# Kernel optimization log

Hardware: AMD Instinct MI355X
Metric: run time of the kernel (lower is better)

The kernel has to match this reference:

```python
import jax, jax.numpy as jnp
import numpy as np

B, H, S, D = 2, 16, 2048, 64


def setup_inputs() -> dict:
    key = jax.random.key(0)
    kq, kk, kv = jax.random.split(key, 3)
    Q = jax.random.normal(kq, (B, H, S, D), dtype=jnp.float32)
    K = jax.random.normal(kk, (B, H, S, D), dtype=jnp.float32)
    V = jax.random.normal(kv, (B, H, S, D), dtype=jnp.float32)
    # causal mask: True = masked out (matches torch masked_fill_ semantics)
    causal = ~jnp.tril(jnp.ones((S, S), dtype=bool))
    mask = jnp.broadcast_to(causal, (B, H, S, S))
    return {"Q": Q, "K": K, "V": V, "mask": mask}


def reference(Q, K, V, mask):
    d_q = Q.shape[-1]
    scale = 1.0 / np.sqrt(d_q).astype(np.float32)
    # scores: (B, H, S, S)
    scores = jnp.einsum('bhqd,bhkd->bhqk', Q, K) * scale
    scores = jnp.where(mask, jnp.float32(-1e9), scores)
    attention = jax.nn.softmax(scores, axis=-1)
    context = jnp.einsum('bhqk,bhkd->bhqd', attention, V)
    return (context, attention)
```

## Files before the change

### kernel.cpp

```cpp
#include <hip/hip_runtime.h>
#include <hip/hip_bf16.h>


constexpr int SEQ = 2048;
constexpr int HD  = 64;
constexpr int NHEADS = 32;
constexpr int QT  = 64;
constexpr int NT  = SEQ / QT;

typedef __bf16 bf16x8 __attribute__((ext_vector_type(8)));
typedef unsigned short u16x8 __attribute__((ext_vector_type(8)));
typedef unsigned short u16x4 __attribute__((ext_vector_type(4)));
typedef float f32x4 __attribute__((ext_vector_type(4)));
typedef unsigned short us;

__device__ __forceinline__ us f2bf(float x) {
  unsigned u = __builtin_bit_cast(unsigned, x);
  return (us)((u + 0x7fffu + ((u >> 16) & 1u)) >> 16);
}
__device__ __forceinline__ float bf2f(us b) {
  return __builtin_bit_cast(float, (unsigned)b << 16);
}

__launch_bounds__(256, 2)
__global__ void attn_kernel(const float* __restrict__ Qg,
                            const float* __restrict__ Kg,
                            const float* __restrict__ Vg,
                            float* __restrict__ out) {
  const int fb = blockIdx.x;
  const int bh = fb & (NHEADS - 1);
  const int pi = fb >> 5;
  const int t  = threadIdx.x;
  const int l  = t & 63;
  const int w  = t >> 6;
  const int l16 = l & 15;
  const int lg  = l >> 4;

  __shared__ __align__(16) us Qs[QT * HD];
  __shared__ __align__(16) us Ks[QT * HD];
  __shared__ __align__(16) us Vs[QT * HD];
  __shared__ __align__(16) us Ps[4][16 * QT];

  const size_t hoff = (size_t)bh * SEQ * HD;
  const float* Qh = Qg + hoff;
  const float* Kh = Kg + hoff;
  const float* Vh = Vg + hoff;
  float* ctx = out + hoff;
  float* att = out + (size_t)NHEADS * SEQ * HD + (size_t)bh * SEQ * SEQ;

  auto load_tile = [&](const float* src, f32x4 (&reg)[4]) {
    #pragma unroll
    for (int j = 0; j < 4; ++j) {
      const int f = t + 256 * j;
      reg[j] = *(const f32x4*)(src + (size_t)(f >> 4) * HD + 4 * (f & 15));
    }
  };
  auto write_k = [&](const f32x4 (&reg)[4], us* dst) {
    #pragma unroll
    for (int j = 0; j < 4; ++j) {
      const int f = t + 256 * j;
      const int r = f >> 4, c4 = f & 15;
      const int idx = (r * 64 + 4 * c4) ^ ((r & 7) << 3);
      u16x4 b = { f2bf(reg[j].x), f2bf(reg[j].y), f2bf(reg[j].z), f2bf(reg[j].w) };
      *(u16x4*)(&dst[idx]) = b;
    }
  };
  auto write_vv = [&](const f32x4 (&reg)[4], us* dst) {
    #pragma unroll
    for (int j = 0; j < 4; ++j) {
      const int f = t + 256 * j;
      const int r = f >> 4, c4 = f & 15;
      const int idx = (r * 64 + 4 * c4) ^ (((r >> 3) & 3) << 4);
      u16x4 b = { f2bf(reg[j].x), f2bf(reg[j].y), f2bf(reg[j].z), f2bf(reg[j].w) };
      *(u16x4*)(&dst[idx]) = b;
    }
  };

  const float sc = 0.125f;

  for (int half = 0; half < 2; ++half) {
    const int qt = half ? (NT - 1 - pi) : pi;
    const int qbase = qt * QT;
    const int qg = qbase + w * 16 + l16;

    __syncthreads();

    {
      const int zc0 = (qt + 1) * QT;
      const int nz4 = (SEQ - zc0) >> 2;
      for (int r = 0; r < QT; ++r) {
        float* rowp = att + (size_t)(qbase + r) * SEQ + zc0;
        for (int c = t; c < nz4; c += 256)
          __builtin_nontemporal_store((f32x4){0.f, 0.f, 0.f, 0.f}, (f32x4*)(rowp + 4 * c));
      }
    }

    {
      f32x4 qreg[4];
      load_tile(Qh + (size_t)qbase * HD, qreg);
      write_k(qreg, Qs);
    }
    __syncthreads();

    bf16x8 aq[2];
    #pragma unroll
    for (int ks = 0; ks < 2; ++ks) {
      const int qr = w * 16 + l16;
      const int d0 = ks * 32 + lg * 8;
      const int idx = (qr * 64 + d0) ^ ((qr & 7) << 3);
      aq[ks] = __builtin_bit_cast(bf16x8, *(const u16x8*)(&Qs[idx]));
    }

    float rsum = 0.f;
    {
      f32x4 kreg[4];
      load_tile(Kh, kreg);
      write_k(kreg, Ks);
      __syncthreads();
      for (int kt = 0; kt <= qt; ++kt) {
        if (kt < qt) load_tile(Kh + (size_t)(kt + 1) * QT * HD, kreg);
        const int kb = kt * QT;
        #pragma unroll
        for (int ct = 0; ct < 4; ++ct) {
          f32x4 acc = {0.f, 0.f, 0.f, 0.f};
          #pragma unroll
          for (int ks = 0; ks < 2; ++ks) {
            const int kr = ct * 16 + l16;
            const int d0 = ks * 32 + lg * 8;
            const int idx = (kr * 64 + d0) ^ ((kr & 7) << 3);
            bf16x8 bk = __builtin_bit_cast(bf16x8, *(const u16x8*)(&Ks[idx]));
            acc = __builtin_amdgcn_mfma_f32_16x16x32_bf16(bk, aq[ks], acc, 0, 0, 0);
          }
          const int kg0 = kb + ct * 16 + lg * 4;
          #pragma unroll
          for (int r = 0; r < 4; ++r) {
            float e = __expf(acc[r] * sc);
            rsum += (kg0 + r <= qg) ? e : 0.f;
          }
        }
        __syncthreads();
        if (kt < qt) write_k(kreg, Ks);
        __syncthreads();
      }
    }
    rsum += __shfl_xor(rsum, 16);
    rsum += __shfl_xor(rsum, 32);
    const float inv = 1.f / rsum;

    f32x4 oacc[4];
    #pragma unroll
    for (int ct = 0; ct < 4; ++ct) oacc[ct] = (f32x4){0.f, 0.f, 0.f, 0.f};

    {
      f32x4 kreg[4], vreg[4];
      load_tile(Kh, kreg);
      load_tile(Vh, vreg);
      write_k(kreg, Ks);
      write_vv(vreg, Vs);
      __syncthreads();
      for (int kt = 0; kt <= qt; ++kt) {
        if (kt < qt) {
          load_tile(Kh + (size_t)(kt + 1) * QT * HD, kreg);
          load_tile(Vh + (size_t)(kt + 1) * QT * HD, vreg);
        }
        const int kb = kt * QT;

        #pragma unroll
        for (int ct = 0; ct < 4; ++ct) {
          f32x4 acc = {0.f, 0.f, 0.f, 0.f};
          #pragma unroll
          for (int ks = 0; ks < 2; ++ks) {
            const int kr = ct * 16 + l16;
            const int d0 = ks * 32 + lg * 8;
            const int idx = (kr * 64 + d0) ^ ((kr & 7) << 3);
            bf16x8 bk = __builtin_bit_cast(bf16x8, *(const u16x8*)(&Ks[idx]));
            acc = __builtin_amdgcn_mfma_f32_16x16x32_bf16(bk, aq[ks], acc, 0, 0, 0);
          }
          const int kg0 = kb + ct * 16 + lg * 4;
          u16x4 pb;
          #pragma unroll
          for (int r = 0; r < 4; ++r) {
            float e = __expf(acc[r] * sc) * inv;
            pb[r] = f2bf((kg0 + r <= qg) ? e : 0.f);
          }
          const int pidx = (l16 * 64 + ct * 16 + lg * 4) ^ ((l16 & 7) << 3);
          *(u16x4*)(&Ps[w][pidx]) = pb;
        }

        #pragma unroll
        for (int ct = 0; ct < 4; ++ct) {
          #pragma unroll
          for (int ks = 0; ks < 2; ++ks) {
            const int key0 = ks * 32 + lg * 8;
            const int pidx = (l16 * 64 + key0) ^ ((l16 & 7) << 3);
            bf16x8 pa = __builtin_bit_cast(bf16x8, *(const u16x8*)(&Ps[w][pidx]));
            bf16x8 av;
            const int dcol = ct * 16 + l16;
            const int xorv = ((key0 >> 3) & 3) << 4;
            #pragma unroll
            for (int j = 0; j < 8; ++j) {
              av[j] = __builtin_bit_cast(__bf16, Vs[((key0 + j) * 64 + dcol) ^ xorv]);
            }
            oacc[ct] = __builtin_amdgcn_mfma_f32_16x16x32_bf16(av, pa, oacc[ct], 0, 0, 0);
          }
        }

        __syncthreads();

        #pragma unroll
        for (int j = 0; j < 4; ++j) {
          const int f = t + 256 * j;
          const int r = f >> 4, c4 = f & 15;
          const int ww = r >> 4, qr = r & 15;
          const int idx = (qr * 64 + 4 * c4) ^ ((qr & 7) << 3);
          u16x4 pb = *(const u16x4*)(&Ps[ww][idx]);
          f32x4 pv = { bf2f(pb[0]), bf2f(pb[1]), bf2f(pb[2]), bf2f(pb[3]) };
          __builtin_nontemporal_store(pv,
              (f32x4*)(att + (size_t)(qbase + r) * SEQ + kb + 4 * c4));
        }

        if (kt < qt) {
          write_k(kreg, Ks);
          write_vv(vreg, Vs);
        }
        __syncthreads();
      }
    }

    #pragma unroll
    for (int ct = 0; ct < 4; ++ct) {
      *(f32x4*)(ctx + (size_t)qg * HD + ct * 16 + lg * 4) = oacc[ct];
    }
  }
}

extern "C" void kernel_launch(void* const* d_in, const int* in_sizes, int n_in,
                              void* d_out, int out_size, void* d_ws, size_t ws_size,
                              hipStream_t stream) {
  const float* Q = (const float*)d_in[0];
  const float* K = (const float*)d_in[1];
  const float* V = (const float*)d_in[2];
  float* out = (float*)d_out;
  attn_kernel<<<dim3(NT / 2 * NHEADS), dim3(256), 0, stream>>>(Q, K, V, out);
}
```

Measured before the change: 153.3 us.

## Pre-convert Q/K/V to swizzled bf16 tiles and stream them via direct-to-LDS loads

Adds a prep kernel that converts Q, K and V to bf16 in the workspace, already in swizzled tile order, with V stored transposed. The main kernel then stages tiles with global_load_lds into double-buffered shared memory, which removes per-iteration fp32 conversion and one barrier. V fragments become single vector reads, and the exponent uses exp2 with a folded constant. The cost is an extra launch and a workspace round trip, and the larger LDS footprint may limit the requested occupancy of 3 blocks per CU. A fallback path is kept for when no workspace is available.

```diff
diff --git a/kernel.cpp b/kernel.cpp
--- a/kernel.cpp
+++ b/kernel.cpp
@@ -22,11 +22,58 @@
   return __builtin_bit_cast(float, (unsigned)b << 16);
 }
 
-__launch_bounds__(256, 2)
-__global__ void attn_kernel(const float* __restrict__ Qg,
+#define GLOAD_LDS(gp, lp)                                                        \
+  __builtin_amdgcn_global_load_lds(                                             \
+      (const __attribute__((address_space(1))) void*)(gp),                      \
+      (__attribute__((address_space(3))) void*)(lp), 16, 0, 0)
+
+__device__ __forceinline__ void stage8k(const us* img, us* lds, int w, int l) {
+  const char* g = (const char*)img + w * 2048 + l * 16;
+  char* s = (char*)lds + w * 2048;
+  GLOAD_LDS(g, s);
+  GLOAD_LDS(g + 1024, s + 1024);
+}
+
+__global__ void prep_kernel(const float* __restrict__ Qg,
                             const float* __restrict__ Kg,
                             const float* __restrict__ Vg,
-                            float* __restrict__ out) {
+                            us* __restrict__ ws) {
+  const int tile = blockIdx.x & (NT - 1);
+  const int bh   = blockIdx.x >> 5;
+  const int t = threadIdx.x;
+  const size_t tOff = ((size_t)bh * SEQ + (size_t)tile * QT) * HD;
+  us* Qi = ws + ((size_t)bh * NT + tile) * 4096;
+  us* Ki = Qi + (size_t)NHEADS * NT * 4096;
+  us* Vi = Ki + (size_t)NHEADS * NT * 4096;
+
+  #pragma unroll
+  for (int g0 = 0; g0 < 2; ++g0) {
+    const int g = t + 256 * g0;
+    const int r = g >> 3, c8 = g & 7;
+    const int cp = (8 * c8) ^ ((r & 7) << 3);
+    const float* qs = Qg + tOff + (size_t)r * HD + cp;
+    const float* ks = Kg + tOff + (size_t)r * HD + cp;
+    u16x8 q, k;
+    #pragma unroll
+    for (int j = 0; j < 8; ++j) { q[j] = f2bf(qs[j]); k[j] = f2bf(ks[j]); }
+    *(u16x8*)(Qi + 8 * g) = q;
+    *(u16x8*)(Ki + 8 * g) = k;
+  }
+  #pragma unroll
+  for (int g0 = 0; g0 < 2; ++g0) {
+    const int g = t + 256 * g0;
+    const int d = g >> 3, k8 = g & 7;
+    const int kp = (8 * k8) ^ ((d & 7) << 3);
+    const float* vs = Vg + tOff + d;
+    u16x8 v;
+    #pragma unroll
+    for (int j = 0; j < 8; ++j) v[j] = f2bf(vs[(size_t)(kp + j) * HD]);
+    *(u16x8*)(Vi + 8 * g) = v;
+  }
+}
+
+__launch_bounds__(256, 3)
+__global__ void attn_main(const us* __restrict__ ws, float* __restrict__ out) {
   const int fb = blockIdx.x;
   const int bh = fb & (NHEADS - 1);
   const int pi = fb >> 5;
@@ -36,6 +83,174 @@
   const int l16 = l & 15;
   const int lg  = l >> 4;
 
+  __shared__ __align__(16) us Qs[4096];
+  __shared__ __align__(16) us Ks[2][4096];
+  __shared__ __align__(16) us Vs[2][4096];
+  __shared__ __align__(16) us Ps[4][1024];
+
+  const us* Qi = ws + (size_t)bh * NT * 4096;
+  const us* Ki = Qi + (size_t)NHEADS * NT * 4096;
+  const us* Vi = Ki + (size_t)NHEADS * NT * 4096;
+
+  float* ctx = out + (size_t)bh * SEQ * HD;
+  float* att = out + (size_t)NHEADS * SEQ * HD + (size_t)bh * SEQ * SEQ;
+
+  const float KC = 0.18033688011112042f;
+
+  for (int half = 0; half < 2; ++half) {
+    const int qt = half ? (NT - 1 - pi) : pi;
+    const int qbase = qt * QT;
+    const int qg = qbase + w * 16 + l16;
+
+    stage8k(Qi + (size_t)qt * 4096, Qs, w, l);
+    stage8k(Ki, Ks[0], w, l);
+    {
+      const int zc0 = (qt + 1) * QT;
+      const int nz4 = (SEQ - zc0) >> 2;
+      for (int r = 0; r < QT; ++r) {
+        float* rowp = att + (size_t)(qbase + r) * SEQ + zc0;
+        for (int c = t; c < nz4; c += 256)
+          __builtin_nontemporal_store((f32x4){0.f, 0.f, 0.f, 0.f}, (f32x4*)(rowp + 4 * c));
+      }
+    }
+    __syncthreads();
+
+    bf16x8 aq[2];
+    #pragma unroll
+    for (int ks = 0; ks < 2; ++ks) {
+      const int qr = w * 16 + l16;
+      const int d0 = ks * 32 + lg * 8;
+      const int idx = (qr * 64 + d0) ^ ((qr & 7) << 3);
+      aq[ks] = __builtin_bit_cast(bf16x8, *(const u16x8*)(&Qs[idx]));
+    }
+
+    float rsum = 0.f;
+    {
+      int cur = 0;
+      for (int kt = 0; kt <= qt; ++kt) {
+        if (kt < qt) stage8k(Ki + (size_t)(kt + 1) * 4096, Ks[cur ^ 1], w, l);
+        const us* krb = Ks[cur];
+        const int kb = kt * QT;
+        #pragma unroll
+        for (int ct = 0; ct < 4; ++ct) {
+          f32x4 acc = {0.f, 0.f, 0.f, 0.f};
+          #pragma unroll
+          for (int ks = 0; ks < 2; ++ks) {
+            const int kr = ct * 16 + l16;
+            const int d0 = ks * 32 + lg * 8;
+            const int idx = (kr * 64 + d0) ^ ((kr & 7) << 3);
+            bf16x8 bk = __builtin_bit_cast(bf16x8, *(const u16x8*)(&krb[idx]));
+            acc = __builtin_amdgcn_mfma_f32_16x16x32_bf16(bk, aq[ks], acc, 0, 0, 0);
+          }
+          const int kg0 = kb + ct * 16 + lg * 4;
+          #pragma unroll
+          for (int r = 0; r < 4; ++r) {
+            float e = __builtin_amdgcn_exp2f(acc[r] * KC);
+            rsum += (kg0 + r <= qg) ? e : 0.f;
+          }
+        }
+        __syncthreads();
+        cur ^= 1;
+      }
+    }
+    stage8k(Ki, Ks[0], w, l);
+    stage8k(Vi, Vs[0], w, l);
+    rsum += __shfl_xor(rsum, 16);
+    rsum += __shfl_xor(rsum, 32);
+    const float inv = 1.f / rsum;
+    __syncthreads();
+
+    f32x4 oacc[4];
+    #pragma unroll
+    for (int ct = 0; ct < 4; ++ct) oacc[ct] = (f32x4){0.f, 0.f, 0.f, 0.f};
+
+    {
+      int cur = 0;
+      for (int kt = 0; kt <= qt; ++kt) {
+        if (kt < qt) {
+          stage8k(Ki + (size_t)(kt + 1) * 4096, Ks[cur ^ 1], w, l);
+          stage8k(Vi + (size_t)(kt + 1) * 4096, Vs[cur ^ 1], w, l);
+        }
+        const us* krb = Ks[cur];
+        const us* vrb = Vs[cur];
+        const int kb = kt * QT;
+
+        #pragma unroll
+        for (int ct = 0; ct < 4; ++ct) {
+          f32x4 acc = {0.f, 0.f, 0.f, 0.f};
+          #pragma unroll
+          for (int ks = 0; ks < 2; ++ks) {
+            const int kr = ct * 16 + l16;
+            const int d0 = ks * 32 + lg * 8;
+            const int idx = (kr * 64 + d0) ^ ((kr & 7) << 3);
+            bf16x8 bk = __builtin_bit_cast(bf16x8, *(const u16x8*)(&krb[idx]));
+            acc = __builtin_amdgcn_mfma_f32_16x16x32_bf16(bk, aq[ks], acc, 0, 0, 0);
+          }
+          const int kg0 = kb + ct * 16 + lg * 4;
+          u16x4 pb;
+          #pragma unroll
+          for (int r = 0; r < 4; ++r) {
+            float e = __builtin_amdgcn_exp2f(acc[r] * KC) * inv;
+            pb[r] = f2bf((kg0 + r <= qg) ? e : 0.f);
+          }
+          const int pidx = (l16 * 64 + ct * 16 + lg * 4) ^ ((l16 & 7) << 3);
+          *(u16x4*)(&Ps[w][pidx]) = pb;
+        }
+
+        #pragma unroll
+        for (int j = 0; j < 4; ++j) {
+          const int rloc = lg + 4 * j;
+          const int idx = (rloc * 64 + 4 * l16) ^ ((rloc & 7) << 3);
+          u16x4 p4 = *(const u16x4*)(&Ps[w][idx]);
+          f32x4 pv = { bf2f(p4[0]), bf2f(p4[1]), bf2f(p4[2]), bf2f(p4[3]) };
+          __builtin_nontemporal_store(pv,
+              (f32x4*)(att + (size_t)(qbase + w * 16 + rloc) * SEQ + kb + 4 * l16));
+        }
+
+        bf16x8 pa[2];
+        #pragma unroll
+        for (int ks = 0; ks < 2; ++ks) {
+          const int pidx = (l16 * 64 + ks * 32 + lg * 8) ^ ((l16 & 7) << 3);
+          pa[ks] = __builtin_bit_cast(bf16x8, *(const u16x8*)(&Ps[w][pidx]));
+        }
+        #pragma unroll
+        for (int ct = 0; ct < 4; ++ct) {
+          #pragma unroll
+          for (int ks = 0; ks < 2; ++ks) {
+            const int dr = ct * 16 + l16;
+            const int key0 = ks * 32 + lg * 8;
+            const int vidx = (dr * 64 + key0) ^ ((dr & 7) << 3);
+            bf16x8 av = __builtin_bit_cast(bf16x8, *(const u16x8*)(&vrb[vidx]));
+            oacc[ct] = __builtin_amdgcn_mfma_f32_16x16x32_bf16(av, pa[ks], oacc[ct], 0, 0, 0);
+          }
+        }
+
+        __syncthreads();
+        cur ^= 1;
+      }
+    }
+
+    #pragma unroll
+    for (int ct = 0; ct < 4; ++ct)
+      __builtin_nontemporal_store(oacc[ct],
+          (f32x4*)(ctx + (size_t)qg * HD + ct * 16 + lg * 4));
+  }
+}
+
+__launch_bounds__(256, 2)
+__global__ void attn_fallback(const float* __restrict__ Qg,
+                              const float* __restrict__ Kg,
+                              const float* __restrict__ Vg,
+                              float* __restrict__ out) {
+  const int fb = blockIdx.x;
+  const int bh = fb & (NHEADS - 1);
+  const int pi = fb >> 5;
+  const int t  = threadIdx.x;
+  const int l  = t & 63;
+  const int w  = t >> 6;
+  const int l16 = l & 15;
+  const int lg  = l >> 4;
+
   __shared__ __align__(16) us Qs[QT * HD];
   __shared__ __align__(16) us Ks[QT * HD];
   __shared__ __align__(16) us Vs[QT * HD];
@@ -84,7 +299,6 @@
     const int qg = qbase + w * 16 + l16;
 
     __syncthreads();
-
     {
       const int zc0 = (qt + 1) * QT;
       const int nz4 = (SEQ - zc0) >> 2;
@@ -94,7 +308,6 @@
           __builtin_nontemporal_store((f32x4){0.f, 0.f, 0.f, 0.f}, (f32x4*)(rowp + 4 * c));
       }
     }
-
     {
       f32x4 qreg[4];
       load_tile(Qh + (size_t)qbase * HD, qreg);
@@ -164,7 +377,6 @@
           load_tile(Vh + (size_t)(kt + 1) * QT * HD, vreg);
         }
         const int kb = kt * QT;
-
         #pragma unroll
         for (int ct = 0; ct < 4; ++ct) {
           f32x4 acc = {0.f, 0.f, 0.f, 0.f};
@@ -186,7 +398,6 @@
           const int pidx = (l16 * 64 + ct * 16 + lg * 4) ^ ((l16 & 7) << 3);
           *(u16x4*)(&Ps[w][pidx]) = pb;
         }
-
         #pragma unroll
         for (int ct = 0; ct < 4; ++ct) {
           #pragma unroll
@@ -198,15 +409,12 @@
             const int dcol = ct * 16 + l16;
             const int xorv = ((key0 >> 3) & 3) << 4;
             #pragma unroll
-            for (int j = 0; j < 8; ++j) {
+            for (int j = 0; j < 8; ++j)
               av[j] = __builtin_bit_cast(__bf16, Vs[((key0 + j) * 64 + dcol) ^ xorv]);
-            }
             oacc[ct] = __builtin_amdgcn_mfma_f32_16x16x32_bf16(av, pa, oacc[ct], 0, 0, 0);
           }
         }
-
-        __syncthreads();
-
+        __syncthreads();
         #pragma unroll
         for (int j = 0; j < 4; ++j) {
           const int f = t + 256 * j;
@@ -218,7 +426,6 @@
           __builtin_nontemporal_store(pv,
               (f32x4*)(att + (size_t)(qbase + r) * SEQ + kb + 4 * c4));
         }
-
         if (kt < qt) {
           write_k(kreg, Ks);
           write_vv(vreg, Vs);
@@ -226,11 +433,9 @@
         __syncthreads();
       }
     }
-
-    #pragma unroll
-    for (int ct = 0; ct < 4; ++ct) {
+    #pragma unroll
+    for (int ct = 0; ct < 4; ++ct)
       *(f32x4*)(ctx + (size_t)qg * HD + ct * 16 + lg * 4) = oacc[ct];
-    }
   }
 }
 
@@ -241,5 +446,12 @@
   const float* K = (const float*)d_in[1];
   const float* V = (const float*)d_in[2];
   float* out = (float*)d_out;
-  attn_kernel<<<dim3(NT / 2 * NHEADS), dim3(256), 0, stream>>>(Q, K, V, out);
-}
+  const size_t NEED = (size_t)3 * NHEADS * NT * 4096 * sizeof(us);
+  if (ws_size >= NEED && d_ws != nullptr) {
+    us* wsp = (us*)d_ws;
+    prep_kernel<<<dim3(NHEADS * NT), dim3(256), 0, stream>>>(Q, K, V, wsp);
+    attn_main<<<dim3(NT / 2 * NHEADS), dim3(256), 0, stream>>>(wsp, out);
+  } else {
+    attn_fallback<<<dim3(NT / 2 * NHEADS), dim3(256), 0, stream>>>(Q, K, V, out);
+  }
+}
```

Result: faster. 142.1 us (-7.4%).
